# Optimization experiments

Hardware: AMD Instinct MI355X
Metric: run time of the kernel (lower is better)

## Reference

```python
import jax, jax.numpy as jnp
import numpy as np

KERNEL_SIZE = 5   # from __init__ default
SIGMA_S = 1.0     # spatial gaussian sigma (both axes)
SIGMA_R = 0.04    # range (color) gaussian sigma


def _space_kernel(k, sigma):
    # kornia-style 1D gaussian, normalized to sum 1, then outer product -> (k, k)
    x = jnp.arange(k, dtype=jnp.float32) - (k // 2)
    g = jnp.exp(-(x * x) / (2.0 * sigma * sigma))
    g = g / g.sum()
    return jnp.outer(g, g)


def setup_inputs() -> dict:
    key = jax.random.key(0)
    images = jax.random.uniform(key, (16, 512, 512, 3), dtype=jnp.float32)  # [B,H,W,3] in [0,1]
    return {"images": images}


def reference(images):
    k = KERNEL_SIZE
    pad = k // 2
    x = jnp.transpose(images, (0, 3, 1, 2))  # (B, C, H, W)
    B, C, H, W = x.shape
    xp = jnp.pad(x, ((0, 0), (0, 0), (pad, pad), (pad, pad)), mode="reflect")
    sk = _space_kernel(k, SIGMA_S).astype(x.dtype)
    inv2sr2 = 0.5 / (SIGMA_R * SIGMA_R)
    num = jnp.zeros_like(x)
    den = jnp.zeros((B, 1, H, W), dtype=x.dtype)
    # fused accumulation over the k*k window (fixed 25-tap loop, fully vectorized per tap)
    for dy in range(k):
        for dx in range(k):
            sh = xp[:, :, dy:dy + H, dx:dx + W]                  # shifted neighbor (B,C,H,W)
            d2 = jnp.sum((sh - x) ** 2, axis=1, keepdims=True)   # color distance^2 (B,1,H,W)
            w = sk[dy, dx] * jnp.exp(-inv2sr2 * d2)              # space * range weight
            num = num + w * sh
            den = den + w
    out = jnp.clip(num / den, 0.0, 1.0)
    return jnp.transpose(out, (0, 2, 3, 1))  # back to (B, H, W, C)
```

## Files before the change

### kernel.cpp

```cpp
#include <hip/hip_runtime.h>
#include <math.h>

#define IMG_H 512
#define IMG_W 512
#define CH    3
#define TILE  16
#define PAD   2
#define TP    (TILE + 2 * PAD)

#if __has_builtin(__builtin_amdgcn_exp2f)
#define EXP2(x) __builtin_amdgcn_exp2f(x)
#else
#define EXP2(x) exp2f(x)
#endif

#if __has_builtin(__builtin_amdgcn_rcpf)
#define RCP(x) __builtin_amdgcn_rcpf(x)
#else
#define RCP(x) (1.0f / (x))
#endif

__device__ __forceinline__ int reflect_idx(int i, int n) {
    i = (i < 0) ? -i : i;
    i = (i >= n) ? (2 * n - 2 - i) : i;
    return i;
}

__global__ __launch_bounds__(256)
void bilateral_kernel(const float* __restrict__ in, float* __restrict__ out) {
    __shared__ float4 lds[TP][TP];

    const float S2   = 312.5f * 1.44269504088896f;
    const float S    = sqrtf(S2);
    const float invS = 1.0f / S;

    const int b  = blockIdx.z;
    const int by = blockIdx.y * TILE;
    const int bx = blockIdx.x * TILE;
    const int tx = threadIdx.x;
    const int ty = threadIdx.y;
    const int tid = ty * TILE + tx;

    for (int i = tid; i < TP * TP; i += 256) {
        const int py = i / TP;
        const int px = i - py * TP;
        const int gy = reflect_idx(by + py - PAD, IMG_H);
        const int gx = reflect_idx(bx + px - PAD, IMG_W);
        const float* src = in + ((size_t)(b * IMG_H + gy) * IMG_W + gx) * CH;
        const float s0 = src[0] * S;
        const float s1 = src[1] * S;
        const float s2 = src[2] * S;
        const float mq = -fmaf(s0, s0, fmaf(s1, s1, s2 * s2));
        ((float4*)lds)[i] = make_float4(s0, s1, s2, mq);
    }
    __syncthreads();

    const float4 c = lds[ty + PAD][tx + PAD];
    const float c20 = c.x + c.x;
    const float c21 = c.y + c.y;
    const float c22 = c.z + c.z;

    const float Cw00 = -8.395800f;
    const float Cw01 = -6.231757f;
    const float Cw02 = -5.510409f;
    const float Cw11 = -4.067714f;
    const float Cw12 = -3.346367f;
    const float Cw22 = -2.625024f;

    const float A[3][3] = {
        { Cw00 + c.w, Cw01 + c.w, Cw02 + c.w },
        { Cw01 + c.w, Cw11 + c.w, Cw12 + c.w },
        { Cw02 + c.w, Cw12 + c.w, Cw22 + c.w },
    };

    float n0 = 0.0f, n1 = 0.0f, n2 = 0.0f, den = 0.0f;

    #pragma unroll
    for (int dy = 0; dy < 5; ++dy) {
        #pragma unroll
        for (int dx = 0; dx < 5; ++dx) {
            const int iy = (dy < 3) ? dy : 4 - dy;
            const int ix = (dx < 3) ? dx : 4 - dx;
            const float4 s = lds[ty + dy][tx + dx];
            const float arg = fmaf(s.x, c20,
                              fmaf(s.y, c21,
                              fmaf(s.z, c22, A[iy][ix] + s.w)));
            const float w = EXP2(arg);
            n0 = fmaf(w, s.x, n0);
            n1 = fmaf(w, s.y, n1);
            n2 = fmaf(w, s.z, n2);
            den += w;
        }
    }

    const float inv = RCP(den * S);
    const int y = by + ty;
    const int x = bx + tx;
    float* dst = out + ((size_t)(b * IMG_H + y) * IMG_W + x) * CH;
    dst[0] = fminf(fmaxf(n0 * inv, 0.0f), 1.0f);
    dst[1] = fminf(fmaxf(n1 * inv, 0.0f), 1.0f);
    dst[2] = fminf(fmaxf(n2 * inv, 0.0f), 1.0f);
}

extern "C" void kernel_launch(void* const* d_in, const int* in_sizes, int n_in,
                              void* d_out, int out_size, void* d_ws, size_t ws_size,
                              hipStream_t stream) {
    const float* in = (const float*)d_in[0];
    float* out = (float*)d_out;
    const int B = in_sizes[0] / (IMG_H * IMG_W * CH);

    dim3 block(TILE, TILE, 1);
    dim3 grid(IMG_W / TILE, IMG_H / TILE, B);
    bilateral_kernel<<<grid, block, 0, stream>>>(in, out);
}
```

Baseline: 40.72 us.

## Compute four output rows per thread with register row reuse and packed FMA

Each thread now computes four vertically adjacent pixels and loads each LDS row once, reusing it across the outputs whose windows cover it. This cuts LDS reads per output and shrinks the halo overhead, since the tile grows to 16x64. The spatial weight is split into separable per-axis constants folded into s.w and a per-row base. Arithmetic uses v2f packed FMAs so the compiler can emit packed fp32 instructions. In exchange, register pressure rises and the grid has a quarter as many blocks.

```diff
diff --git a/kernel.cpp b/kernel.cpp
--- a/kernel.cpp
+++ b/kernel.cpp
@@ -4,9 +4,15 @@
 #define IMG_H 512
 #define IMG_W 512
 #define CH    3
-#define TILE  16
+#define BX    16
+#define TY    16
+#define PPT   4
+#define TILE_H (TY * PPT)
 #define PAD   2
-#define TP    (TILE + 2 * PAD)
+#define TPW   (BX + 2 * PAD)
+#define TPH   (TILE_H + 2 * PAD)
+
+typedef float v2f __attribute__((ext_vector_type(2)));
 
 #if __has_builtin(__builtin_amdgcn_exp2f)
 #define EXP2(x) __builtin_amdgcn_exp2f(x)
@@ -28,22 +34,20 @@
 
 __global__ __launch_bounds__(256)
 void bilateral_kernel(const float* __restrict__ in, float* __restrict__ out) {
-    __shared__ float4 lds[TP][TP];
+    __shared__ float4 lds[TPH][TPW];
 
-    const float S2   = 312.5f * 1.44269504088896f;
-    const float S    = sqrtf(S2);
-    const float invS = 1.0f / S;
+    const float S = sqrtf(312.5f * 1.44269504088896f);
 
     const int b  = blockIdx.z;
-    const int by = blockIdx.y * TILE;
-    const int bx = blockIdx.x * TILE;
+    const int by = blockIdx.y * TILE_H;
+    const int bx = blockIdx.x * BX;
     const int tx = threadIdx.x;
     const int ty = threadIdx.y;
-    const int tid = ty * TILE + tx;
+    const int tid = ty * BX + tx;
 
-    for (int i = tid; i < TP * TP; i += 256) {
-        const int py = i / TP;
-        const int px = i - py * TP;
+    for (int i = tid; i < TPH * TPW; i += 256) {
+        const int py = i / TPW;
+        const int px = i - py * TPW;
         const int gy = reflect_idx(by + py - PAD, IMG_H);
         const int gx = reflect_idx(bx + px - PAD, IMG_W);
         const float* src = in + ((size_t)(b * IMG_H + gy) * IMG_W + gx) * CH;
@@ -51,55 +55,70 @@
         const float s1 = src[1] * S;
         const float s2 = src[2] * S;
         const float mq = -fmaf(s0, s0, fmaf(s1, s1, s2 * s2));
-        ((float4*)lds)[i] = make_float4(s0, s1, s2, mq);
+        lds[py][px] = make_float4(s0, s1, s2, mq);
     }
     __syncthreads();
 
-    const float4 c = lds[ty + PAD][tx + PAD];
-    const float c20 = c.x + c.x;
-    const float c21 = c.y + c.y;
-    const float c22 = c.z + c.z;
+    const float CW[3] = { -4.1978935f, -2.0338538f, -1.3125121f };
 
-    const float Cw00 = -8.395800f;
-    const float Cw01 = -6.231757f;
-    const float Cw02 = -5.510409f;
-    const float Cw11 = -4.067714f;
-    const float Cw12 = -3.346367f;
-    const float Cw22 = -2.625024f;
+    const int ty4 = ty * PPT;
 
-    const float A[3][3] = {
-        { Cw00 + c.w, Cw01 + c.w, Cw02 + c.w },
-        { Cw01 + c.w, Cw11 + c.w, Cw12 + c.w },
-        { Cw02 + c.w, Cw12 + c.w, Cw22 + c.w },
-    };
+    v2f   c01[PPT];
+    v2f   c2z1[PPT];
+    float cw[PPT];
+    #pragma unroll
+    for (int j = 0; j < PPT; ++j) {
+        const float4 c = lds[ty4 + j + PAD][tx + PAD];
+        c01[j]  = (v2f){ c.x + c.x, c.y + c.y };
+        c2z1[j] = (v2f){ c.z + c.z, 1.0f };
+        cw[j]   = c.w;
+    }
 
-    float n0 = 0.0f, n1 = 0.0f, n2 = 0.0f, den = 0.0f;
+    v2f   nxy[PPT];
+    float n2[PPT], den[PPT];
+    #pragma unroll
+    for (int j = 0; j < PPT; ++j) {
+        nxy[j] = (v2f){ 0.0f, 0.0f };
+        n2[j] = 0.0f; den[j] = 0.0f;
+    }
 
     #pragma unroll
-    for (int dy = 0; dy < 5; ++dy) {
+    for (int r = 0; r < PPT + 4; ++r) {
+        float4 s[5];
         #pragma unroll
-        for (int dx = 0; dx < 5; ++dx) {
-            const int iy = (dy < 3) ? dy : 4 - dy;
-            const int ix = (dx < 3) ? dx : 4 - dx;
-            const float4 s = lds[ty + dy][tx + dx];
-            const float arg = fmaf(s.x, c20,
-                              fmaf(s.y, c21,
-                              fmaf(s.z, c22, A[iy][ix] + s.w)));
-            const float w = EXP2(arg);
-            n0 = fmaf(w, s.x, n0);
-            n1 = fmaf(w, s.y, n1);
-            n2 = fmaf(w, s.z, n2);
-            den += w;
+        for (int k = 0; k < 5; ++k) {
+            s[k] = lds[ty4 + r][tx + k];
+            s[k].w += CW[k < 3 ? k : 4 - k];
+        }
+        #pragma unroll
+        for (int j = 0; j < PPT; ++j) {
+            const int dy = r - j;
+            if (dy < 0 || dy > 4) continue;
+            const float base = cw[j] + CW[dy < 3 ? dy : 4 - dy];
+            const v2f base0 = (v2f){ base, 0.0f };
+            #pragma unroll
+            for (int k = 0; k < 5; ++k) {
+                const v2f sxy = (v2f){ s[k].x, s[k].y };
+                const v2f szw = (v2f){ s[k].z, s[k].w };
+                const v2f q = __builtin_elementwise_fma(szw, c2z1[j], base0);
+                const v2f p = __builtin_elementwise_fma(sxy, c01[j], q);
+                const float w = EXP2(p.x + p.y);
+                nxy[j] = __builtin_elementwise_fma((v2f){ w, w }, sxy, nxy[j]);
+                n2[j]  = fmaf(w, s[k].z, n2[j]);
+                den[j] += w;
+            }
         }
     }
 
-    const float inv = RCP(den * S);
-    const int y = by + ty;
-    const int x = bx + tx;
-    float* dst = out + ((size_t)(b * IMG_H + y) * IMG_W + x) * CH;
-    dst[0] = fminf(fmaxf(n0 * inv, 0.0f), 1.0f);
-    dst[1] = fminf(fmaxf(n1 * inv, 0.0f), 1.0f);
-    dst[2] = fminf(fmaxf(n2 * inv, 0.0f), 1.0f);
+    #pragma unroll
+    for (int j = 0; j < PPT; ++j) {
+        const float inv = RCP(den[j] * S);
+        const int y = by + ty4 + j;
+        float* dst = out + ((size_t)(b * IMG_H + y) * IMG_W + (bx + tx)) * CH;
+        dst[0] = fminf(fmaxf(nxy[j].x * inv, 0.0f), 1.0f);
+        dst[1] = fminf(fmaxf(nxy[j].y * inv, 0.0f), 1.0f);
+        dst[2] = fminf(fmaxf(n2[j]  * inv, 0.0f), 1.0f);
+    }
 }
 
 extern "C" void kernel_launch(void* const* d_in, const int* in_sizes, int n_in,
@@ -109,7 +128,7 @@
     float* out = (float*)d_out;
     const int B = in_sizes[0] / (IMG_H * IMG_W * CH);
 
-    dim3 block(TILE, TILE, 1);
-    dim3 grid(IMG_W / TILE, IMG_H / TILE, B);
+    dim3 block(BX, TY, 1);
+    dim3 grid(IMG_W / BX, IMG_H / TILE_H, B);
     bilateral_kernel<<<grid, block, 0, stream>>>(in, out);
 }
```

New measurement: 51.66 us. +26.9%, slower.
